# Optimization experiments

Measured on AMD Instinct MI355X. Metric: run time of the kernel, lower is better.

The kernel has to match this reference:

```python
import jax, jax.numpy as jnp
import numpy as np
from itertools import permutations, combinations

BATCH = 32768
EPS = 1e-06  # positivity eps from __init__


def _levi_civita7():
    e = np.zeros((7,) * 7, dtype=np.float32)
    for p in permutations(range(7)):
        inv = sum(1 for i in range(7) for j in range(i + 1, 7) if p[i] > p[j])
        e[p] = -1.0 if inv % 2 else 1.0
    return jnp.asarray(e)

_EPS7 = _levi_civita7()  # (7,7,7,7,7,7,7) rank-7 Levi-Civita tensor
_TRIPLES = np.array(list(combinations(range(7), 3)), dtype=np.int32)  # (35,3) i<j<k index triples
_PERMS3 = [((0, 1, 2), 1.0), ((1, 2, 0), 1.0), ((2, 0, 1), 1.0),
           ((0, 2, 1), -1.0), ((2, 1, 0), -1.0), ((1, 0, 2), -1.0)]


def _phi_full(phi):
    # expand 35 independent components to fully antisymmetric (B,7,7,7)
    b = phi.shape[0]
    pf = jnp.zeros((b, 7, 7, 7), phi.dtype)
    for perm, s in _PERMS3:
        ia = _TRIPLES[:, perm[0]]
        ib = _TRIPLES[:, perm[1]]
        ic = _TRIPLES[:, perm[2]]
        pf = pf.at[:, ia, ib, ic].set(s * phi)
    return pf


def _metric_from_phi(phi):
    # Standard G2 metric: B_ij = (1/144) phi_ikl phi_jmn phi_pqr eps^{klmnpqr};
    # g = B / |det B|^{1/9}  (unit-determinant normalization)
    pf = _phi_full(phi)  # (B,7,7,7)
    C = jnp.einsum('klmnpqr,bpqr->bklmn', _EPS7, pf)  # (B,7,7,7,7)
    T = jnp.einsum('bklmn,bjmn->bklj', C, pf)          # (B,7,7,7)
    Bm = jnp.einsum('bikl,bklj->bij', pf, T) / 144.0   # (B,7,7)
    det = jnp.linalg.det(Bm)
    g = Bm / (jnp.abs(det)[:, None, None] + 1e-12) ** (1.0 / 9.0)
    return 0.5 * (g + jnp.swapaxes(g, -1, -2))  # exact symmetry for eigvalsh


def setup_inputs() -> dict:
    key = jax.random.key(0)
    phi = jax.random.normal(key, (BATCH, 35), dtype=jnp.float32)
    return {"phi": phi}


def reference(phi):
    g = _metric_from_phi(phi)              # (B,7,7)
    ev = jnp.linalg.eigvalsh(g)            # (B,7)
    return jax.nn.relu(-ev + EPS).sum(axis=-1)  # (B,) sum of negative-eigenvalue violations
```

## Files before the change

kernel.cpp:

```cpp
#include <hip/hip_runtime.h>
#include <utility>

#define BATCH 32768
#define NPHI 35

typedef float v2f __attribute__((ext_vector_type(2)));

constexpr int choose2(int n){ return (n*(n-1))/2; }

constexpr int tri_id_sorted(int a,int b,int c){
  int id=0;
  for(int x=0;x<a;++x) id += choose2(6-x);
  for(int y=a+1;y<b;++y) id += (6-y);
  id += (c-b-1);
  return id;
}

constexpr int tri_id3(int a,int b,int c){
  int x=a,y=b,z=c;
  if (x>y){int t=x;x=y;y=t;}
  if (y>z){int t=y;y=z;z=t;}
  if (x>y){int t=x;x=y;y=t;}
  return tri_id_sorted(x,y,z);
}

constexpr int sgn3(int a,int b,int c){
  int inv = (a>b)+(a>c)+(b>c);
  return (inv&1)? -1 : 1;
}

constexpr int UT(int i,int j){
  return i*7 - (i*(i-1))/2 + (j-i);
}

constexpr int PAIR(int k,int l){
  return k*7 - (k*(k+1))/2 + (l - k - 1);
}

struct Prog {
  int n;
  unsigned char kind[1472];
  unsigned char init[1472];
  short         dst [1472];
  unsigned char a   [1472];
  short         b   [1472];
  signed char   s   [1472];
};

constexpr Prog build_prog(){
  Prog P{}; P.n=0;
  bool uinit[28]={};
  for(int k=0;k<7;++k) for(int l=k+1;l<7;++l){
    const int kl = PAIR(k,l);
    bool tinit[7]={};
    for(int m=0;m<7;++m) for(int n2=m+1;n2<7;++n2){
      if(m==k||m==l||n2==k||n2==l) continue;
      int comp[3]={0,0,0}; int cn=0;
      for(int x=0;x<7;++x) if(x!=k&&x!=l&&x!=m&&x!=n2){ comp[cn]=x; ++cn; }
      int perm[7]={k,l,m,n2,comp[0],comp[1],comp[2]};
      int invc=0;
      for(int i=0;i<7;++i) for(int j=i+1;j<7;++j) if(perm[i]>perm[j]) ++invc;
      const int es=(invc&1)? -1 : 1;
      const int tcomp=tri_id_sorted(comp[0],comp[1],comp[2]);
      for(int j=0;j<7;++j){
        if(j==m||j==n2) continue;
        P.kind[P.n]=0;
        P.init[P.n]=tinit[j]?0:1; tinit[j]=true;
        P.dst [P.n]=(short)(kl*7+j);
        P.a   [P.n]=(unsigned char)tcomp;
        P.b   [P.n]=(short)tri_id3(j,m,n2);
        P.s   [P.n]=(signed char)(es*sgn3(j,m,n2));
        ++P.n;
      }
    }
    for(int i=0;i<7;++i){
      if(i==k||i==l) continue;
      for(int j=i;j<7;++j){
        P.kind[P.n]=1;
        P.init[P.n]=uinit[UT(i,j)]?0:1; uinit[UT(i,j)]=true;
        P.dst [P.n]=(short)UT(i,j);
        P.a   [P.n]=(unsigned char)tri_id3(i,k,l);
        P.b   [P.n]=(short)(kl*7+j);
        P.s   [P.n]=(signed char)sgn3(i,k,l);
        ++P.n;
      }
    }
  }
  return P;
}

static constexpr Prog PROG = build_prog();
static_assert(PROG.n == 1470, "program size unexpected");

template<int Q>
__device__ __forceinline__ void step(float (&T)[147], float (&U)[28],
                                     const float (&ph)[NPHI]){
  constexpr int  d = PROG.dst[Q];
  constexpr int  a = PROG.a[Q];
  constexpr int  b = PROG.b[Q];
  constexpr bool neg  = (PROG.s[Q] < 0);
  constexpr bool init = (PROG.init[Q] != 0);
  if constexpr (PROG.kind[Q] == 0){
    const float x = neg ? -ph[a] : ph[a];
    if constexpr (init) T[d] = x * ph[b];
    else                T[d] = fmaf(x, ph[b], T[d]);
  } else {
    const float x = neg ? -ph[a] : ph[a];
    if constexpr (init) U[d] = x * T[b];
    else                U[d] = fmaf(x, T[b], U[d]);
  }
}

template<int... Q>
__device__ __forceinline__ void run_prog(float (&T)[147], float (&U)[28],
                                         const float (&ph)[NPHI],
                                         std::integer_sequence<int, Q...>){
  (step<Q>(T, U, ph), ...);
}

__global__ __launch_bounds__(64,1)
void PositivityConstraint_89086211654295_kernel(const float* __restrict__ phi,
                                                float* __restrict__ out){
  const int gid = blockIdx.x*64 + threadIdx.x;

  const float* __restrict__ p = phi + (size_t)gid * NPHI;
  float ph[NPHI];
  {
    const float4* __restrict__ p4 = reinterpret_cast<const float4*>(p);
    #pragma unroll
    for (int k=0;k<8;++k){
      const float4 v = p4[k];
      ph[4*k+0]=v.x; ph[4*k+1]=v.y; ph[4*k+2]=v.z; ph[4*k+3]=v.w;
    }
    ph[32]=p[32]; ph[33]=p[33]; ph[34]=p[34];
  }

  float T[147];
  float U[28];
  run_prog(T, U, ph, std::make_integer_sequence<int, PROG.n>{});

  float A[28];
  #pragma unroll
  for (int i=0;i<28;++i) A[i] = U[i]*(1.0f/6.0f);

  #pragma unroll 1
  for (int sweep=0; sweep<6; ++sweep){
    #pragma unroll
    for (int p1=0;p1<7;++p1){
      #pragma unroll
      for (int q1=p1+1;q1<7;++q1){
        const float apq = A[UT(p1,q1)];
        const float app = A[UT(p1,p1)];
        const float aqq = A[UT(q1,q1)];
        if (__any(fabsf(apq) > 1e-7f*(fabsf(app)+fabsf(aqq)))) {
          float d = 2.0f*apq;
          d = d + ((d >= 0.0f)? 1e-30f : -1e-30f);
          const float tau = (aqq - app) * __builtin_amdgcn_rcpf(d);
          float t = __builtin_amdgcn_rcpf(
                      fabsf(tau) + __builtin_amdgcn_sqrtf(fmaf(tau,tau,1.0f)));
          t = (tau >= 0.0f)? t : -t;
          const float c = __builtin_amdgcn_rsqf(fmaf(t,t,1.0f));
          const float s = t*c;
          A[UT(p1,p1)] = fmaf(-t, apq, app);
          A[UT(q1,q1)] = fmaf( t, apq, aqq);
          A[UT(p1,q1)] = 0.0f;
          const v2f cs  = {  c, s };
          const v2f msc = { -s, c };
          #pragma unroll
          for (int r=0;r<7;++r){
            if (r==p1 || r==q1) continue;
            const int irp = (r<p1)? UT(r,p1) : UT(p1,r);
            const int irq = (r<q1)? UT(r,q1) : UT(q1,r);
            const v2f arp2 = { A[irp], A[irp] };
            const v2f arq2 = { A[irq], A[irq] };
            const v2f res = __builtin_elementwise_fma(cs, arp2, msc*arq2);
            A[irp] = res.x;
            A[irq] = res.y;
          }
        }
      }
    }
  }

  float det = 1.0f;
  #pragma unroll
  for (int i=0;i<7;++i) det *= A[UT(i,i)];
  const float ad = fabsf(det) + 1e-12f;
  const float scale = __builtin_amdgcn_exp2f(__builtin_amdgcn_logf(ad) * (1.0f/9.0f));
  const float inv = __builtin_amdgcn_rcpf(scale);

  float sum = 0.0f;
  #pragma unroll
  for (int i=0;i<7;++i){
    const float ev = A[UT(i,i)]*inv;
    const float r = 1e-6f - ev;
    sum += fmaxf(r, 0.0f);
  }
  out[gid] = sum;
}

extern "C" void kernel_launch(void* const* d_in, const int* in_sizes, int n_in,
                              void* d_out, int out_size, void* d_ws, size_t ws_size,
                              hipStream_t stream) {
  const float* phi = (const float*)d_in[0];
  float* out = (float*)d_out;
  (void)in_sizes; (void)n_in; (void)out_size; (void)d_ws; (void)ws_size;
  hipLaunchKernelGGL(PositivityConstraint_89086211654295_kernel,
                     dim3(BATCH/64), dim3(64), 0, stream, phi, out);
}
```

Measured before the change: 66.52 us.

## Cut Jacobi sweeps, drop per-rotation guards, add sched barriers between phases

Cuts the Jacobi eigenvalue iteration from six sweeps to four unguarded sweeps plus one final guarded sweep, and loosens the skip threshold in that last sweep. This removes the wave-wide vote and branch on every rotation in most sweeps and cuts the total rotation work. It also inserts scheduling barriers wherever the contraction program switches between the T and U phases, and after the program ends, to limit register pressure from compiler interleaving. The trade-off is fewer sweeps, which risks less accurate eigenvalues for slowly converging matrices.

```diff
diff --git a/kernel.cpp b/kernel.cpp
--- a/kernel.cpp
+++ b/kernel.cpp
@@ -95,6 +95,9 @@
 template<int Q>
 __device__ __forceinline__ void step(float (&T)[147], float (&U)[28],
                                      const float (&ph)[NPHI]){
+  if constexpr (Q > 0 && PROG.kind[Q] != PROG.kind[Q-1]) {
+    __builtin_amdgcn_sched_barrier(0);
+  }
   constexpr int  d = PROG.dst[Q];
   constexpr int  a = PROG.a[Q];
   constexpr int  b = PROG.b[Q];
@@ -118,6 +121,41 @@
   (step<Q>(T, U, ph), ...);
 }
 
+#define ROT_BODY(p1, q1, GUARD)                                               \
+  {                                                                           \
+    const float apq = A[UT(p1,q1)];                                           \
+    const float app = A[UT(p1,p1)];                                           \
+    const float aqq = A[UT(q1,q1)];                                           \
+    bool doit = true;                                                         \
+    if (GUARD) doit = __any(fabsf(apq) > 1e-6f*(fabsf(app)+fabsf(aqq)));      \
+    if (doit) {                                                               \
+      float d = 2.0f*apq;                                                     \
+      d = d + ((d >= 0.0f)? 1e-30f : -1e-30f);                                \
+      const float tau = (aqq - app) * __builtin_amdgcn_rcpf(d);               \
+      float t = __builtin_amdgcn_rcpf(                                        \
+                  fabsf(tau) + __builtin_amdgcn_sqrtf(fmaf(tau,tau,1.0f)));   \
+      t = (tau >= 0.0f)? t : -t;                                              \
+      const float c = __builtin_amdgcn_rsqf(fmaf(t,t,1.0f));                  \
+      const float s = t*c;                                                    \
+      A[UT(p1,p1)] = fmaf(-t, apq, app);                                      \
+      A[UT(q1,q1)] = fmaf( t, apq, aqq);                                      \
+      A[UT(p1,q1)] = 0.0f;                                                    \
+      const v2f cs  = {  c, s };                                              \
+      const v2f msc = { -s, c };                                              \
+      _Pragma("unroll")                                                       \
+      for (int r=0;r<7;++r){                                                  \
+        if (r==p1 || r==q1) continue;                                         \
+        const int irp = (r<p1)? UT(r,p1) : UT(p1,r);                          \
+        const int irq = (r<q1)? UT(r,q1) : UT(q1,r);                          \
+        const v2f arp2 = { A[irp], A[irp] };                                  \
+        const v2f arq2 = { A[irq], A[irq] };                                  \
+        const v2f res = __builtin_elementwise_fma(cs, arp2, msc*arq2);        \
+        A[irp] = res.x;                                                       \
+        A[irq] = res.y;                                                       \
+      }                                                                       \
+    }                                                                         \
+  }
+
 __global__ __launch_bounds__(64,1)
 void PositivityConstraint_89086211654295_kernel(const float* __restrict__ phi,
                                                 float* __restrict__ out){
@@ -138,46 +176,28 @@
   float T[147];
   float U[28];
   run_prog(T, U, ph, std::make_integer_sequence<int, PROG.n>{});
+  __builtin_amdgcn_sched_barrier(0);
 
   float A[28];
   #pragma unroll
   for (int i=0;i<28;++i) A[i] = U[i]*(1.0f/6.0f);
 
   #pragma unroll 1
-  for (int sweep=0; sweep<6; ++sweep){
+  for (int sweep=0; sweep<4; ++sweep){
     #pragma unroll
     for (int p1=0;p1<7;++p1){
       #pragma unroll
       for (int q1=p1+1;q1<7;++q1){
-        const float apq = A[UT(p1,q1)];
-        const float app = A[UT(p1,p1)];
-        const float aqq = A[UT(q1,q1)];
-        if (__any(fabsf(apq) > 1e-7f*(fabsf(app)+fabsf(aqq)))) {
-          float d = 2.0f*apq;
-          d = d + ((d >= 0.0f)? 1e-30f : -1e-30f);
-          const float tau = (aqq - app) * __builtin_amdgcn_rcpf(d);
-          float t = __builtin_amdgcn_rcpf(
-                      fabsf(tau) + __builtin_amdgcn_sqrtf(fmaf(tau,tau,1.0f)));
-          t = (tau >= 0.0f)? t : -t;
-          const float c = __builtin_amdgcn_rsqf(fmaf(t,t,1.0f));
-          const float s = t*c;
-          A[UT(p1,p1)] = fmaf(-t, apq, app);
-          A[UT(q1,q1)] = fmaf( t, apq, aqq);
-          A[UT(p1,q1)] = 0.0f;
-          const v2f cs  = {  c, s };
-          const v2f msc = { -s, c };
-          #pragma unroll
-          for (int r=0;r<7;++r){
-            if (r==p1 || r==q1) continue;
-            const int irp = (r<p1)? UT(r,p1) : UT(p1,r);
-            const int irq = (r<q1)? UT(r,q1) : UT(q1,r);
-            const v2f arp2 = { A[irp], A[irp] };
-            const v2f arq2 = { A[irq], A[irq] };
-            const v2f res = __builtin_elementwise_fma(cs, arp2, msc*arq2);
-            A[irp] = res.x;
-            A[irq] = res.y;
-          }
-        }
+        ROT_BODY(p1, q1, false)
+      }
+    }
+  }
+  {
+    #pragma unroll
+    for (int p1=0;p1<7;++p1){
+      #pragma unroll
+      for (int q1=p1+1;q1<7;++q1){
+        ROT_BODY(p1, q1, true)
       }
     }
   }
```

Result: faster. 62.44 us (-6.1%).
